# Kernel tuning notes

Measured on AMD Instinct MI355X. Metric: run time of the kernel, lower is better.

## Reference

```python
import jax, jax.numpy as jnp
import numpy as np
from jax import lax

B, C, H, W = 8, 256, 64, 64
O, K, E = 256, 3, 3  # out_channels, kernel_size, num_experts

def setup_inputs() -> dict:
    key = jax.random.key(0)
    k1, k2, k3, k4, k5 = jax.random.split(key, 5)
    q = jax.random.normal(k1, (B, C, H, W), dtype=jnp.float32)
    y = jax.random.normal(k2, (B, C, H, W), dtype=jnp.float32)
    experts = jax.random.normal(k3, (E, O, 2 * C, K, K), dtype=jnp.float32)
    # torch nn.Linear(2C, E): store transposed [2C, E] for ctx @ gate_w
    bound = 1.0 / np.sqrt(2 * C)
    gate_w = jax.random.uniform(k4, (2 * C, E), minval=-bound, maxval=bound, dtype=jnp.float32)
    gate_b = jax.random.uniform(k5, (E,), minval=-bound, maxval=bound, dtype=jnp.float32)
    return {"q": q, "y": y, "experts": experts, "gate_w": gate_w, "gate_b": gate_b}

def reference(q, y, experts, gate_w, gate_b):
    # gate: softmax over experts from global-avg-pooled context of y (duplicated)
    y_ctx = jnp.mean(y, axis=(2, 3))                       # [B, C]
    context = jnp.concatenate([y_ctx, y_ctx], axis=1)       # [B, 2C]
    gates = jax.nn.softmax(context @ gate_w + gate_b, axis=1)  # [B, E]
    # per-sample fused kernel: sum_e gates[b,e] * experts[e]  -> [B, O, 2C, K, K]
    w = jnp.einsum('be,eoikl->boikl', gates, experts)
    xy = jnp.concatenate([q, q], axis=1)                     # [B, 2C, H, W]
    # batched dynamic conv via grouped conv: batch -> groups (no Python loop)
    b, c2, h, wd = xy.shape
    x1 = xy.reshape(1, b * c2, h, wd)
    w1 = w.reshape(b * O, c2, K, K)
    out = lax.conv_general_dilated(
        x1, w1, window_strides=(1, 1), padding='SAME',
        dimension_numbers=('NCHW', 'OIHW', 'NCHW'),
        feature_group_count=b)
    return out.reshape(b, O, h, wd)
```

## Files before the change

kernel.cpp:

```cpp
#include <hip/hip_runtime.h>
#include <hip/hip_bf16.h>
#include <math.h>


typedef __bf16 bf16x8 __attribute__((ext_vector_type(8)));
typedef __bf16 bf16x4 __attribute__((ext_vector_type(4)));
typedef float f32x4 __attribute__((ext_vector_type(4)));

#define AS1 __attribute__((address_space(1)))
#define AS3 __attribute__((address_space(3)))

__global__ __launch_bounds__(256) void yctx_kernel(const float* __restrict__ y,
                                                   float* __restrict__ yctx) {
  int bc = blockIdx.x;
  const float4* p = (const float4*)(y + (size_t)bc * 4096);
  int tid = threadIdx.x;
  float s = 0.f;
#pragma unroll
  for (int k = 0; k < 4; k++) {
    float4 v = p[tid + k * 256];
    s += v.x + v.y + v.z + v.w;
  }
#pragma unroll
  for (int off = 32; off > 0; off >>= 1) s += __shfl_down(s, off, 64);
  __shared__ float wsum[4];
  if ((tid & 63) == 0) wsum[tid >> 6] = s;
  __syncthreads();
  if (tid == 0) yctx[bc] = (wsum[0] + wsum[1] + wsum[2] + wsum[3]) * (1.f / 4096.f);
}

union PrepSmem {
  struct {
    float sfold[3 * 16 * 145];
    float lg[8][3];
    float g[8][3];
  } wb;
  float tile2[64][33];
};

__global__ __launch_bounds__(256) void prep_kernel(const float* __restrict__ q,
                                                   const float* __restrict__ experts,
                                                   const float* __restrict__ yctx,
                                                   const float* __restrict__ gw,
                                                   const float* __restrict__ gb,
                                                   __bf16* __restrict__ qT,
                                                   __bf16* __restrict__ wf) {
  __shared__ PrepSmem sm;
  int bid = blockIdx.x;
  int tid = threadIdx.x;

  if (bid < 256) {
    int og = bid >> 4, chh = bid & 15;
    int chb = chh >> 1;
    int qb = (chh & 1) * 2;

    {
      int lb = tid >> 5, li = tid & 31;
      float p0 = 0.f, p1 = 0.f, p2 = 0.f;
#pragma unroll
      for (int j = 0; j < 8; j++) {
        int c = li + j * 32;
        float yv = yctx[lb * 256 + c];
        p0 += yv * (gw[c * 3 + 0] + gw[(c + 256) * 3 + 0]);
        p1 += yv * (gw[c * 3 + 1] + gw[(c + 256) * 3 + 1]);
        p2 += yv * (gw[c * 3 + 2] + gw[(c + 256) * 3 + 2]);
      }
#pragma unroll
      for (int off = 16; off > 0; off >>= 1) {
        p0 += __shfl_down(p0, off, 32);
        p1 += __shfl_down(p1, off, 32);
        p2 += __shfl_down(p2, off, 32);
      }
      if (li == 0) {
        sm.wb.lg[lb][0] = p0 + gb[0];
        sm.wb.lg[lb][1] = p1 + gb[1];
        sm.wb.lg[lb][2] = p2 + gb[2];
      }
    }

    for (int i = tid; i < 1728; i += 256) {
      int p = i / 36, f = i - p * 36;
      int e = p >> 4, olp = p & 15;
      int o = og * 16 + olp;
      const float4* src = (const float4*)experts + ((size_t)(e * 256 + o)) * 1152 + chh * 36;
      float4 lo = src[f], hi = src[f + 576];
      float* dst = &sm.wb.sfold[p * 145 + f * 4];
      dst[0] = lo.x + hi.x; dst[1] = lo.y + hi.y;
      dst[2] = lo.z + hi.z; dst[3] = lo.w + hi.w;
    }
    __syncthreads();
    if (tid < 8) {
      float l0 = sm.wb.lg[tid][0], l1 = sm.wb.lg[tid][1], l2 = sm.wb.lg[tid][2];
      float m = fmaxf(l0, fmaxf(l1, l2));
      float e0 = __expf(l0 - m), e1 = __expf(l1 - m), e2 = __expf(l2 - m);
      float inv = 1.f / (e0 + e1 + e2);
      sm.wb.g[tid][0] = e0 * inv; sm.wb.g[tid][1] = e1 * inv; sm.wb.g[tid][2] = e2 * inv;
    }
    __syncthreads();

#pragma unroll 1
    for (int b = 0; b < 8; b++) {
      float g0 = sm.wb.g[b][0], g1 = sm.wb.g[b][1], g2 = sm.wb.g[b][2];
      for (int i = tid; i < 288; i += 256) {
        int tap = i >> 5, ck = i & 31;
        int qdl = ck >> 4, ol = ck & 15;
        const float* r0 = &sm.wb.sfold[(0 * 16 + ol) * 145 + (qdl * 8) * 9 + tap];
        const float* r1 = &sm.wb.sfold[(1 * 16 + ol) * 145 + (qdl * 8) * 9 + tap];
        const float* r2 = &sm.wb.sfold[(2 * 16 + ol) * 145 + (qdl * 8) * 9 + tap];
        bf16x8 rv;
#pragma unroll
        for (int j = 0; j < 8; j++) {
          float v = g0 * r0[j * 9] + g1 * r1[j * 9] + g2 * r2[j * 9];
          rv[j] = (__bf16)v;
        }
        size_t byteoff = (((size_t)b * 9 + tap) * 8 + chb) * 16384 +
                         (size_t)og * 1024 + (size_t)(qb + qdl) * 256 + (size_t)ol * 16;
        *(bf16x8*)((char*)wf + byteoff) = rv;
      }
    }
    return;
  }

  int bid2 = bid - 256;
  int hp = bid2 % 66;
  int t2 = bid2 / 66;
  int ch = t2 & 7;
  int b = t2 >> 3;
  __bf16* dst = qT + (((size_t)(b * 8 + ch) * 66 + hp) * 66) * 32;
  float4 z4 = {0.f, 0.f, 0.f, 0.f};
  if (hp == 0 || hp == 65) {
    float4* d4 = (float4*)dst;
    for (int i = tid; i < 264; i += 256) d4[i] = z4;
    return;
  }
  int h = hp - 1;
  {
    int w = tid & 63, ci = tid >> 6;
#pragma unroll
    for (int j = 0; j < 8; j++) {
      int c = ci * 8 + j;
      sm.tile2[w][c] = q[(((size_t)b * 256 + ch * 32 + c) * 64 + h) * 64 + w];
    }
  }
  if (tid < 4) ((float4*)dst)[tid] = z4;
  else if (tid < 8) ((float4*)(dst + 65 * 32))[tid - 4] = z4;
  __syncthreads();

  int a = tid & 7, wsl = tid >> 3;
  int cl4 = a * 4;
#pragma unroll
  for (int k = 0; k < 2; k++) {
    int w = wsl * 2 + k, wp = w + 1;
    int clp4 = (((cl4 >> 3) ^ ((wp >> 1) & 3)) << 3) | (cl4 & 7);
    float v0 = sm.tile2[w][cl4 + 0], v1 = sm.tile2[w][cl4 + 1];
    float v2 = sm.tile2[w][cl4 + 2], v3 = sm.tile2[w][cl4 + 3];
    bf16x4 r = {(__bf16)v0, (__bf16)v1, (__bf16)v2, (__bf16)v3};
    *(bf16x4*)(dst + wp * 32 + clp4) = r;
  }
}

__global__ __launch_bounds__(512, 2) void conv_kernel(const __bf16* __restrict__ qT,
                                                      const __bf16* __restrict__ wf,
                                                      float* __restrict__ out) {
  __shared__ __align__(16) __bf16 Qlds[2][6 * 66 * 32];
  const int tid = threadIdx.x;
  const int lane = tid & 63;
  const int wv = tid >> 6;
  const int wm = wv >> 2;
  const int wn = wv & 3;
  const int l15 = lane & 15, qd = lane >> 4;

  const int bid = blockIdx.x;
  const int b = bid & 7;
  const int rem = bid >> 3;
  const int o0 = (rem >> 4) * 128;
  const int hq = (rem & 15) * 4;

  f32x4 acc[4][4];
  {
    f32x4 z = {0.f, 0.f, 0.f, 0.f};
#pragma unroll
    for (int i = 0; i < 4; i++)
#pragma unroll
      for (int j = 0; j < 4; j++) acc[i][j] = z;
  }

  const char* qT_b = (const char*)qT + (size_t)b * 8 * 66 * 66 * 32 * 2;
  const char* abase = (const char*)wf + (size_t)b * 9 * 8 * 16384 +
                      (size_t)(o0 + wm * 64) * 64 + (size_t)lane * 16;
  bf16x8 areg[3][4];

  {
    const char* qsrc = qT_b + ((size_t)hq) * 66 * 32 * 2;
    for (int i = tid; i < 1584; i += 512) {
      int ub = i - lane;
      __builtin_amdgcn_global_load_lds((const AS1 void*)(qsrc + ((size_t)i << 4)),
                                       (AS3 void*)((char*)Qlds[0] + ((size_t)ub << 4)),
                                       16, 0, 0);
    }
#pragma unroll
    for (int mi = 0; mi < 4; mi++) {
      areg[0][mi] = *(const bf16x8*)(abase + mi * 1024);
      areg[1][mi] = *(const bf16x8*)(abase + ((size_t)8 << 14) + mi * 1024);
    }
    __syncthreads();
  }

#pragma unroll 1
  for (int ch = 0; ch < 8; ch++) {
    const char* Qb = (const char*)Qlds[ch & 1];
    const char* qsrc_n = qT_b + ((size_t)(ch + 1) * 66 + hq) * 66 * 32 * 2;
    char* qdst_n = (char*)Qlds[(ch + 1) & 1];
#pragma unroll
    for (int tap = 0; tap < 9; tap++) {
      {
        int tapn = (tap + 2 >= 9) ? tap - 7 : tap + 2;
        int chn = (tap + 2 >= 9) ? ch + 1 : ch;
        size_t aoff = ((size_t)(tapn * 8 + chn)) << 14;
#pragma unroll
        for (int mi = 0; mi < 4; mi++)
          areg[(tap + 2) % 3][mi] = *(const bf16x8*)(abase + aoff + mi * 1024);
      }
      if (ch < 7) {
        if (tap == 0) {
          for (int i = tid; i < 792; i += 512) {
            int ub = i - lane;
            __builtin_amdgcn_global_load_lds((const AS1 void*)(qsrc_n + ((size_t)i << 4)),
                                             (AS3 void*)(qdst_n + ((size_t)ub << 4)),
                                             16, 0, 0);
          }
        } else if (tap == 1) {
          for (int i = 792 + tid; i < 1584; i += 512) {
            int ub = i - lane;
            __builtin_amdgcn_global_load_lds((const AS1 void*)(qsrc_n + ((size_t)i << 4)),
                                             (AS3 void*)(qdst_n + ((size_t)ub << 4)),
                                             16, 0, 0);
          }
        }
      }
      const int dh = tap / 3, dw = tap - dh * 3;
      const int r = wn + dh;
#pragma unroll
      for (int ni = 0; ni < 4; ni++) {
        int wp = ni * 16 + l15 + dw;
        int g = (qd ^ ((wp >> 1) & 3)) << 3;
        bf16x8 bfv = *(const bf16x8*)(Qb + ((r * 66 + wp) * 32 + g) * 2);
#pragma unroll
        for (int mi = 0; mi < 4; mi++)
          acc[mi][ni] = __builtin_amdgcn_mfma_f32_16x16x32_bf16(
              areg[tap % 3][mi], bfv, acc[mi][ni], 0, 0, 0);
      }
    }
    __syncthreads();
  }

  const int hh = hq + wn;
#pragma unroll
  for (int mi = 0; mi < 4; mi++) {
    int o = o0 + wm * 64 + mi * 16 + qd * 4;
#pragma unroll
    for (int ni = 0; ni < 4; ni++) {
      int w = ni * 16 + l15;
#pragma unroll
      for (int rr = 0; rr < 4; rr++)
        out[(((size_t)b * 256 + (o + rr)) * 64 + hh) * 64 + w] = acc[mi][ni][rr];
    }
  }
}

extern "C" void kernel_launch(void* const* d_in, const int* in_sizes, int n_in,
                              void* d_out, int out_size, void* d_ws, size_t ws_size,
                              hipStream_t stream) {
  (void)in_sizes; (void)n_in; (void)out_size; (void)ws_size;
  const float* q = (const float*)d_in[0];
  const float* y = (const float*)d_in[1];
  const float* experts = (const float*)d_in[2];
  const float* gate_w = (const float*)d_in[3];
  const float* gate_b = (const float*)d_in[4];
  float* out = (float*)d_out;

  char* ws = (char*)d_ws;
  float* yctx = (float*)ws;
  __bf16* wf = (__bf16*)(ws + 16384);
  __bf16* qT = (__bf16*)(ws + 16384 + 9437184);

  yctx_kernel<<<2048, 256, 0, stream>>>(y, yctx);
  prep_kernel<<<256 + 4224, 256, 0, stream>>>(q, experts, yctx, gate_w, gate_b, qT, wf);
  conv_kernel<<<256, 512, 0, stream>>>(qT, wf, out);
}
```

Before: 158.4 us.

## Process eight rows per block in q transpose with double-buffered LDS prefetch

The q transpose/pad part of the prep kernel now gives each block eight rows instead of one, cutting the grid from 4224 to 512 transpose blocks. Loads for the next row go into registers while the current row is converted and stored from a double-buffered LDS tile. Stores are widened to 16-byte bf16x8, and each store writes the zero padding columns itself. This aims to cut launch and per-block overhead and hide global load latency, at the cost of fewer blocks in flight and a serial per-row loop with syncs.

```diff
diff --git a/kernel.cpp b/kernel.cpp
--- a/kernel.cpp
+++ b/kernel.cpp
@@ -35,7 +35,7 @@
     float lg[8][3];
     float g[8][3];
   } wb;
-  float tile2[64][33];
+  float t2[2][64][33];
 };
 
 __global__ __launch_bounds__(256) void prep_kernel(const float* __restrict__ q,
@@ -121,41 +121,67 @@
     return;
   }
 
-  int bid2 = bid - 256;
-  int hp = bid2 % 66;
-  int t2 = bid2 / 66;
-  int ch = t2 & 7;
-  int b = t2 >> 3;
-  __bf16* dst = qT + (((size_t)(b * 8 + ch) * 66 + hp) * 66) * 32;
-  float4 z4 = {0.f, 0.f, 0.f, 0.f};
-  if (hp == 0 || hp == 65) {
-    float4* d4 = (float4*)dst;
-    for (int i = tid; i < 264; i += 256) d4[i] = z4;
-    return;
-  }
-  int h = hp - 1;
   {
+    int qb2 = bid - 256;
+    int hg = qb2 & 7;
+    int t2i = qb2 >> 3;
+    int ch = t2i & 7;
+    int b = t2i >> 3;
+    __bf16* dstbase = qT + ((size_t)(b * 8 + ch) * 66) * 66 * 32;
+    const float* qsrc = q + ((size_t)b * 256 + ch * 32) * 4096;
+
     int w = tid & 63, ci = tid >> 6;
+    int h0r = hg * 8;
 #pragma unroll
     for (int j = 0; j < 8; j++) {
       int c = ci * 8 + j;
-      sm.tile2[w][c] = q[(((size_t)b * 256 + ch * 32 + c) * 64 + h) * 64 + w];
-    }
-  }
-  if (tid < 4) ((float4*)dst)[tid] = z4;
-  else if (tid < 8) ((float4*)(dst + 65 * 32))[tid - 4] = z4;
-  __syncthreads();
-
-  int a = tid & 7, wsl = tid >> 3;
-  int cl4 = a * 4;
-#pragma unroll
-  for (int k = 0; k < 2; k++) {
-    int w = wsl * 2 + k, wp = w + 1;
-    int clp4 = (((cl4 >> 3) ^ ((wp >> 1) & 3)) << 3) | (cl4 & 7);
-    float v0 = sm.tile2[w][cl4 + 0], v1 = sm.tile2[w][cl4 + 1];
-    float v2 = sm.tile2[w][cl4 + 2], v3 = sm.tile2[w][cl4 + 3];
-    bf16x4 r = {(__bf16)v0, (__bf16)v1, (__bf16)v2, (__bf16)v3};
-    *(bf16x4*)(dst + wp * 32 + clp4) = r;
+      sm.t2[0][w][c] = qsrc[((size_t)c * 64 + h0r) * 64 + w];
+    }
+    __syncthreads();
+
+#pragma unroll 1
+    for (int r = 0; r < 8; r++) {
+      float nxt[8];
+      if (r < 7) {
+        int h = h0r + r + 1;
+#pragma unroll
+        for (int j = 0; j < 8; j++) {
+          int c = ci * 8 + j;
+          nxt[j] = qsrc[((size_t)c * 64 + h) * 64 + w];
+        }
+      }
+      int hp = h0r + r + 1;
+      char* dst = (char*)(dstbase + (size_t)hp * 2112);
+      const float (*tcur)[33] = sm.t2[r & 1];
+      for (int m = tid; m < 264; m += 256) {
+        int wp = m >> 2, gp = m & 3;
+        bf16x8 rv;
+        if (wp == 0 || wp == 65) {
+#pragma unroll
+          for (int j = 0; j < 8; j++) rv[j] = (__bf16)0.f;
+        } else {
+          int gsrc = gp ^ ((wp >> 1) & 3);
+          const float* s = &tcur[wp - 1][gsrc * 8];
+#pragma unroll
+          for (int j = 0; j < 8; j++) rv[j] = (__bf16)s[j];
+        }
+        *(bf16x8*)(dst + m * 16) = rv;
+      }
+      if (r < 7) {
+#pragma unroll
+        for (int j = 0; j < 8; j++) {
+          int c = ci * 8 + j;
+          sm.t2[(r + 1) & 1][w][c] = nxt[j];
+        }
+      }
+      __syncthreads();
+    }
+    if (hg == 0 || hg == 7) {
+      int hp = (hg == 0) ? 0 : 65;
+      float4* dz = (float4*)(dstbase + (size_t)hp * 2112);
+      float4 z4 = {0.f, 0.f, 0.f, 0.f};
+      for (int i = tid; i < 264; i += 256) dz[i] = z4;
+    }
   }
 }
 
@@ -285,6 +311,6 @@
   __bf16* qT = (__bf16*)(ws + 16384 + 9437184);
 
   yctx_kernel<<<2048, 256, 0, stream>>>(y, yctx);
-  prep_kernel<<<256 + 4224, 256, 0, stream>>>(q, experts, yctx, gate_w, gate_b, qT, wf);
+  prep_kernel<<<256 + 512, 256, 0, stream>>>(q, experts, yctx, gate_w, gate_b, qT, wf);
   conv_kernel<<<256, 512, 0, stream>>>(qT, wf, out);
 }
```

New measurement: 161.1 us. No clear change (+1.7%).
